# Kernel optimization log

Hardware: AMD Instinct MI355X
Metric: run time of the kernel (lower is better)

The kernel has to match this reference:

```python
import jax, jax.numpy as jnp
import numpy as np

EMB = 1024
NH = 16
T = 2048
B = 2

def setup_inputs() -> dict:
    key = jax.random.key(0)
    k1, k2, k3, k4, k5 = jax.random.split(key, 5)
    s = 0.02
    return {
        "x": jax.random.normal(k1, (B, T, EMB), dtype=jnp.float32),
        "W_attn": jax.random.normal(k2, (EMB, 3 * EMB), dtype=jnp.float32) * s,
        "b_attn": jax.random.normal(k3, (3 * EMB,), dtype=jnp.float32) * s,
        "W_proj": jax.random.normal(k4, (EMB, EMB), dtype=jnp.float32) * s,
        "b_proj": jax.random.normal(k5, (EMB,), dtype=jnp.float32) * s,
    }

def reference(x, W_attn, b_attn, W_proj, b_proj):
    Bz, Tz, C = x.shape
    hd = C // NH
    qkv = x @ W_attn + b_attn                      # [B,T,3C]
    q, k, v = jnp.split(qkv, 3, axis=-1)
    # [B,T,C] -> [B,H,T,hd]
    def heads(t):
        return t.reshape(Bz, Tz, NH, hd).transpose(0, 2, 1, 3)
    q, k, v = heads(q), heads(k), heads(v)
    scale = 1.0 / jnp.sqrt(jnp.float32(hd))
    att = jnp.einsum("bhqd,bhkd->bhqk", q, k) * scale   # [B,H,T,T]
    causal = jnp.tril(jnp.ones((Tz, Tz), dtype=bool))
    att = jnp.where(causal, att, jnp.finfo(att.dtype).min)
    att = jax.nn.softmax(att, axis=-1)
    y = jnp.einsum("bhqk,bhkd->bhqd", att, v)            # [B,H,T,hd]
    y = y.transpose(0, 2, 1, 3).reshape(Bz, Tz, C)
    return y @ W_proj + b_proj
```

## Files before the change

### kernel.cpp

```cpp
#include <hip/hip_runtime.h>
#include <cstdint>
#include <cstddef>

typedef _Float16 half8 __attribute__((ext_vector_type(8)));
typedef _Float16 half4v __attribute__((ext_vector_type(4)));
typedef float f32x4 __attribute__((ext_vector_type(4)));
typedef int int4v __attribute__((ext_vector_type(4)));

#define EMBD 1024
#define NHEAD 16
#define TSEQ 2048
#define NB 2
#define HD 64
#define NBH (NB*NHEAD)
#define SCK 0.18033688f

static __device__ __forceinline__ void gload_lds16(const void* g, void* l) {
    __builtin_amdgcn_global_load_lds((const __attribute__((address_space(1))) void*)g,
                                     (__attribute__((address_space(3))) void*)l,
                                     16, 0, 0);
}

static __device__ __forceinline__ int pk2(float a, float b) {
    return __builtin_bit_cast(int, __builtin_amdgcn_cvt_pkrtz(a, b));
}

__global__ __launch_bounds__(256) void k_prep(
    const float* __restrict__ x,  _Float16* __restrict__ xh,
    const float* __restrict__ Wa, const float* __restrict__ Wp,
    _Float16* __restrict__ WaT,   _Float16* __restrict__ WpT)
{
    const int bx = blockIdx.x;
    if (bx < 4096) {
        int i = bx * 256 + threadIdx.x;
        float4 v = ((const float4*)x)[i];
        half4v h;
        h.x = (_Float16)v.x; h.y = (_Float16)v.y; h.z = (_Float16)v.z; h.w = (_Float16)v.w;
        ((half4v*)xh)[i] = h;
        return;
    }
    __shared__ float tile[32][33];
    const int idx = bx - 4096;
    const int bxx = idx & 127;
    const int byy = idx >> 7;
    const bool isA = bxx < 96;
    const float* in  = isA ? Wa : Wp;
    _Float16* out    = isA ? WaT : WpT;
    const int C      = isA ? 3072 : 1024;
    const int c0 = (isA ? bxx : bxx - 96) * 32, r0 = byy * 32;
    const int tx = threadIdx.x & 31, ty = threadIdx.x >> 5;
    #pragma unroll
    for (int j = 0; j < 4; ++j)
        tile[ty + 8*j][tx] = in[(size_t)(r0 + ty + 8*j) * C + c0 + tx];
    __syncthreads();
    #pragma unroll
    for (int j = 0; j < 4; ++j)
        out[(size_t)(c0 + ty + 8*j) * 1024 + r0 + tx] = (_Float16)tile[tx][ty + 8*j];
}

__global__ __launch_bounds__(256) void k_gemm_qkv(
    const _Float16* __restrict__ A,
    const _Float16* __restrict__ Bt,
    const float* __restrict__ bias,
    _Float16* __restrict__ outq,
    _Float16* __restrict__ VT)
{
    __shared__ _Float16 smem[12288];
    _Float16* As = smem;
    _Float16* Bs = smem + 8192;

    const int d    = blockIdx.x;
    const int xcd  = d & 7;
    const int idx  = d >> 3;
    const int mt   = (xcd >> 1) * 8  + (idx & 7);
    const int ntl  = (xcd &  1) * 24 + (idx >> 3);
    const int m0 = mt * 128, n0 = ntl * 64;

    const int tid  = threadIdx.x;
    const int lane = tid & 63;
    const int w    = tid >> 6;
    const int wm   = w >> 1, wn = w & 1;
    const int l15  = lane & 15;
    const int lg   = lane >> 4;

    f32x4 acc[4][2];
    #pragma unroll
    for (int i = 0; i < 4; ++i) {
        acc[i][0] = (f32x4){0.f, 0.f, 0.f, 0.f};
        acc[i][1] = (f32x4){0.f, 0.f, 0.f, 0.f};
    }

    for (int kt = 0; kt < 16; ++kt) {
        __syncthreads();
        #pragma unroll
        for (int c = 0; c < 4; ++c) {
            int s = c * 256 + tid;
            int r = s >> 3, sl = s & 7;
            const _Float16* ga = A + (size_t)(m0 + r) * 1024 + kt * 64 + ((sl ^ (r & 7)) * 8);
            gload_lds16(ga, (char*)As + s * 16);
        }
        #pragma unroll
        for (int c = 0; c < 2; ++c) {
            int s = c * 256 + tid;
            int r = s >> 3, sl = s & 7;
            const _Float16* gb = Bt + (size_t)(n0 + r) * 1024 + kt * 64 + ((sl ^ (r & 7)) * 8);
            gload_lds16(gb, (char*)Bs + s * 16);
        }
        __syncthreads();

        half8 af[4][2], bf[2][2];
        #pragma unroll
        for (int mf = 0; mf < 4; ++mf) {
            int r = wm * 64 + mf * 16 + l15;
            #pragma unroll
            for (int ks = 0; ks < 2; ++ks)
                af[mf][ks] = *(const half8*)((const char*)As + r * 128 + (((ks * 4 + lg) ^ (r & 7)) * 16));
        }
        #pragma unroll
        for (int nf = 0; nf < 2; ++nf) {
            int r = wn * 32 + nf * 16 + l15;
            #pragma unroll
            for (int ks = 0; ks < 2; ++ks)
                bf[nf][ks] = *(const half8*)((const char*)Bs + r * 128 + (((ks * 4 + lg) ^ (r & 7)) * 16));
        }
        #pragma unroll
        for (int mf = 0; mf < 4; ++mf)
            #pragma unroll
            for (int nf = 0; nf < 2; ++nf) {
                acc[mf][nf] = __builtin_amdgcn_mfma_f32_16x16x32_f16(af[mf][0], bf[nf][0], acc[mf][nf], 0, 0, 0);
                acc[mf][nf] = __builtin_amdgcn_mfma_f32_16x16x32_f16(af[mf][1], bf[nf][1], acc[mf][nf], 0, 0, 0);
            }
    }

    float bv[2];
    bv[0] = bias[n0 + wn * 32 + l15];
    bv[1] = bias[n0 + wn * 32 + 16 + l15];

    const int which = n0 >> 10;
    if (which < 2) {
        const float osc = (which == 1) ? SCK : 1.0f;
        #pragma unroll
        for (int mf = 0; mf < 4; ++mf) {
            #pragma unroll
            for (int j = 0; j < 4; ++j) {
                int m = m0 + wm * 64 + mf * 16 + lg * 4 + j;
                _Float16* po = outq + (size_t)m * 3072 + n0 + wn * 32 + l15;
                po[0]  = (_Float16)((acc[mf][0][j] + bv[0]) * osc);
                po[16] = (_Float16)((acc[mf][1][j] + bv[1]) * osc);
            }
        }
    } else {
        __syncthreads();
        #pragma unroll
        for (int mf = 0; mf < 4; ++mf)
            #pragma unroll
            for (int j = 0; j < 4; ++j) {
                int m = wm * 64 + mf * 16 + lg * 4 + j;
                smem[m * 65 + wn * 32 + l15]      = (_Float16)(acc[mf][0][j] + bv[0]);
                smem[m * 65 + wn * 32 + 16 + l15] = (_Float16)(acc[mf][1][j] + bv[1]);
            }
        __syncthreads();

        const int b     = m0 >> 11;
        const int h     = (n0 - 2048) >> 6;
        const int tloc0 = m0 & 2047;
        _Float16* vbase = VT + ((size_t)(b * 16 + h) * 64) * 2048 + tloc0;
        #pragma unroll
        for (int c = 0; c < 4; ++c) {
            int seg = c * 256 + tid;
            int dd  = seg >> 4;
            int s   = seg & 15;
            half8 hv8;
            #pragma unroll
            for (int e = 0; e < 8; ++e) {
                int p = s * 8 + e;
                int k = 16 * (2 * (p >> 5) + ((p & 7) >> 2)) + 4 * ((p >> 3) & 3) + (p & 3);
                hv8[e] = smem[k * 65 + dd];
            }
            *(half8*)&vbase[(size_t)dd * 2048 + s * 8] = hv8;
        }
    }
}

__global__ __launch_bounds__(256) void k_gemm_proj(
    const _Float16* __restrict__ A,
    const _Float16* __restrict__ Bt,
    const float* __restrict__ bias,
    float* __restrict__ outf)
{
    __shared__ _Float16 As[64 * 64];
    __shared__ _Float16 Bs[128 * 64];

    const int d   = blockIdx.x;
    const int xcd = d & 7;
    const int idx = d >> 3;
    const int mt  = (xcd >> 1) * 16 + (idx & 15);
    const int nt  = (xcd &  1) * 4  + (idx >> 4);
    const int m0 = mt * 64, n0 = nt * 128;

    const int tid  = threadIdx.x;
    const int lane = tid & 63;
    const int wn   = tid >> 6;
    const int l15  = lane & 15;
    const int lg   = lane >> 4;

    f32x4 acc[4][2];
    #pragma unroll
    for (int i = 0; i < 4; ++i) {
        acc[i][0] = (f32x4){0.f, 0.f, 0.f, 0.f};
        acc[i][1] = (f32x4){0.f, 0.f, 0.f, 0.f};
    }

    for (int kt = 0; kt < 16; ++kt) {
        __syncthreads();
        #pragma unroll
        for (int c = 0; c < 2; ++c) {
            int s = c * 256 + tid;
            int r = s >> 3, sl = s & 7;
            const _Float16* ga = A + (size_t)(m0 + r) * 1024 + kt * 64 + ((sl ^ (r & 7)) * 8);
            gload_lds16(ga, (char*)As + s * 16);
        }
        #pragma unroll
        for (int c = 0; c < 4; ++c) {
            int s = c * 256 + tid;
            int r = s >> 3, sl = s & 7;
            const _Float16* gb = Bt + (size_t)(n0 + r) * 1024 + kt * 64 + ((sl ^ (r & 7)) * 8);
            gload_lds16(gb, (char*)Bs + s * 16);
        }
        __syncthreads();

        half8 af[4][2], bf[2][2];
        #pragma unroll
        for (int mf = 0; mf < 4; ++mf) {
            int r = mf * 16 + l15;
            #pragma unroll
            for (int ks = 0; ks < 2; ++ks)
                af[mf][ks] = *(const half8*)((const char*)As + r * 128 + (((ks * 4 + lg) ^ (r & 7)) * 16));
        }
        #pragma unroll
        for (int nf = 0; nf < 2; ++nf) {
            int r = wn * 32 + nf * 16 + l15;
            #pragma unroll
            for (int ks = 0; ks < 2; ++ks)
                bf[nf][ks] = *(const half8*)((const char*)Bs + r * 128 + (((ks * 4 + lg) ^ (r & 7)) * 16));
        }
        #pragma unroll
        for (int mf = 0; mf < 4; ++mf)
            #pragma unroll
            for (int nf = 0; nf < 2; ++nf) {
                acc[mf][nf] = __builtin_amdgcn_mfma_f32_16x16x32_f16(af[mf][0], bf[nf][0], acc[mf][nf], 0, 0, 0);
                acc[mf][nf] = __builtin_amdgcn_mfma_f32_16x16x32_f16(af[mf][1], bf[nf][1], acc[mf][nf], 0, 0, 0);
            }
    }

    float bv[2];
    bv[0] = bias[n0 + wn * 32 + l15];
    bv[1] = bias[n0 + wn * 32 + 16 + l15];

    #pragma unroll
    for (int mf = 0; mf < 4; ++mf) {
        #pragma unroll
        for (int j = 0; j < 4; ++j) {
            int m = m0 + mf * 16 + lg * 4 + j;
            float* po = outf + (size_t)m * 1024 + n0 + wn * 32 + l15;
            po[0]  = acc[mf][0][j] + bv[0];
            po[16] = acc[mf][1][j] + bv[1];
        }
    }
}

__global__ __launch_bounds__(512) void k_attn(
    const _Float16* __restrict__ qkv,
    const _Float16* __restrict__ VTg,
    _Float16* __restrict__ Y)
{
    __shared__ _Float16 Kt[2][8192];
    __shared__ _Float16 Vt[2][8192];

    const int tid  = threadIdx.x;
    const int lane = tid & 63;
    const int w    = tid >> 6;
    const int l15  = lane & 15;
    const int lg   = lane >> 4;
    const int bh   = blockIdx.x;
    const int by   = blockIdx.y;
    const int qt   = (by < 8) ? (15 - by) : (by - 8);
    const int b    = bh >> 4, h = bh & 15;

    const int rA  = tid >> 3;
    const int slA = tid & 7;
    const size_t kOffA = (size_t)rA * 3072 + ((slA ^ (rA & 7)) * 8);
    const _Float16* kBase = qkv + (size_t)(b * 2048) * 3072 + 1024 + h * 64;

    const int dA = tid >> 4;
    const int sA = tid & 15;
    const size_t vOffA = (size_t)dA * 2048 + ((sA ^ (dA & 15)) * 8);
    const _Float16* vBase = VTg + (size_t)bh * TSEQ * HD;

    const int x7   = l15 & 7;
    const int kph0 = (lg ^ x7) * 8;
    const int kph1 = ((4 + lg) ^ x7) * 8;

    const int qrow = qt * 128 + w * 16 + l15;
    const _Float16* qptr = qkv + (size_t)(b * 2048 + qrow) * 3072 + h * 64;
    half8 qa0 = *(const half8*)&qptr[lg * 8];
    half8 qa1 = *(const half8*)&qptr[32 + lg * 8];

    half8 ones;
    #pragma unroll
    for (int i = 0; i < 8; ++i) ones[i] = (_Float16)1.0f;

    f32x4 yac[4];
    #pragma unroll
    for (int nf = 0; nf < 4; ++nf) yac[nf] = (f32x4){0.f, 0.f, 0.f, 0.f};
    f32x4 lsum = (f32x4){0.f, 0.f, 0.f, 0.f};

    const int nkt = qt + 1;

    half8 kra = *(const half8*)(kBase + kOffA);
    half8 krb = *(const half8*)(kBase + kOffA + (size_t)64 * 3072);
    half8 vra = *(const half8*)(vBase + vOffA);
    half8 vrb = *(const half8*)(vBase + vOffA + 32 * 2048);

    for (int kt = 0; kt < nkt; ++kt) {
        const int cur = kt & 1;
        _Float16* KtC = Kt[cur];
        _Float16* VtC = Vt[cur];
        *(half8*)&KtC[tid * 8]        = kra;
        *(half8*)&KtC[4096 + tid * 8] = krb;
        *(half8*)&VtC[tid * 8]        = vra;
        *(half8*)&VtC[4096 + tid * 8] = vrb;
        if (kt + 1 < nkt) {
            const _Float16* kp = kBase + (size_t)(kt + 1) * 128 * 3072;
            kra = *(const half8*)(kp + kOffA);
            krb = *(const half8*)(kp + kOffA + (size_t)64 * 3072);
            const _Float16* vp = vBase + (kt + 1) * 128;
            vra = *(const half8*)(vp + vOffA);
            vrb = *(const half8*)(vp + vOffA + 32 * 2048);
        }
        asm volatile("s_waitcnt lgkmcnt(0)" ::: "memory");
        __builtin_amdgcn_s_barrier();
        __builtin_amdgcn_sched_barrier(0);

        const bool diag = (kt == nkt - 1);

        f32x4 s[8];
        __builtin_amdgcn_s_setprio(1);
        #pragma unroll
        for (int f = 0; f < 8; ++f) {
            if (diag && f > w) { s[f] = (f32x4){0.f, 0.f, 0.f, 0.f}; continue; }
            int rr = f * 16 + l15;
            half8 kb0 = *(const half8*)&KtC[rr * 64 + kph0];
            half8 kb1 = *(const half8*)&KtC[rr * 64 + kph1];
            f32x4 z = (f32x4){0.f, 0.f, 0.f, 0.f};
            z = __builtin_amdgcn_mfma_f32_16x16x32_f16(kb0, qa0, z, 0, 0, 0);
            z = __builtin_amdgcn_mfma_f32_16x16x32_f16(kb1, qa1, z, 0, 0, 0);
            s[f] = z;
        }
        __builtin_amdgcn_s_setprio(0);

        if (diag) {
            const int qg = qt * 128 + w * 16 + l15;
            #pragma unroll
            for (int f = 0; f < 8; ++f) {
                if (f > w) continue;
                #pragma unroll
                for (int j = 0; j < 4; ++j) {
                    int kk = kt * 128 + 16 * f + 4 * lg + j;
                    s[f][j] = (kk > qg) ? 0.f : exp2f(s[f][j]);
                }
            }
        } else {
            #pragma unroll
            for (int f = 0; f < 8; ++f)
                #pragma unroll
                for (int j = 0; j < 4; ++j) s[f][j] = exp2f(s[f][j]);
        }

        __builtin_amdgcn_s_setprio(1);
        #pragma unroll
        for (int t = 0; t < 4; ++t) {
            int4v pi;
            pi[0] = pk2(s[2 * t][0],     s[2 * t][1]);
            pi[1] = pk2(s[2 * t][2],     s[2 * t][3]);
            pi[2] = pk2(s[2 * t + 1][0], s[2 * t + 1][1]);
            pi[3] = pk2(s[2 * t + 1][2], s[2 * t + 1][3]);
            half8 pa = __builtin_bit_cast(half8, pi);
            lsum = __builtin_amdgcn_mfma_f32_16x16x32_f16(pa, ones, lsum, 0, 0, 0);
            #pragma unroll
            for (int nf = 0; nf < 4; ++nf) {
                half8 vb = *(const half8*)&VtC[(nf * 16 + l15) * 128 + (((t * 4 + lg) ^ l15) * 8)];
                yac[nf] = __builtin_amdgcn_mfma_f32_16x16x32_f16(pa, vb, yac[nf], 0, 0, 0);
            }
        }
        __builtin_amdgcn_s_setprio(0);
    }

    const int trow = qt * 128 + w * 16 + lg * 4;
    #pragma unroll
    for (int j = 0; j < 4; ++j) {
        float inv = 1.f / lsum[j];
        #pragma unroll
        for (int nf = 0; nf < 4; ++nf) {
            float yv = yac[nf][j] * inv;
            Y[((size_t)b * TSEQ + trow + j) * EMBD + h * 64 + nf * 16 + l15] = (_Float16)yv;
        }
    }
}

extern "C" void kernel_launch(void* const* d_in, const int* in_sizes, int n_in,
                              void* d_out, int out_size, void* d_ws, size_t ws_size,
                              hipStream_t stream) {
    const float* x  = (const float*)d_in[0];
    const float* Wa = (const float*)d_in[1];
    const float* ba = (const float*)d_in[2];
    const float* Wp = (const float*)d_in[3];
    const float* bp = (const float*)d_in[4];
    float* out = (float*)d_out;

    _Float16* Xh   = (_Float16*)d_ws;
    _Float16* WaT  = Xh   + (size_t)4096 * 1024;
    _Float16* WpT  = WaT  + (size_t)3072 * 1024;
    _Float16* QKVn = WpT  + (size_t)1024 * 1024;
    _Float16* VTb  = QKVn + (size_t)4096 * 3072;
    _Float16* Yh   = Xh;

    k_prep<<<8192, 256, 0, stream>>>(x, Xh, Wa, Wp, WaT, WpT);

    k_gemm_qkv<<<1536, 256, 0, stream>>>(Xh, WaT, ba, QKVn, VTb);

    k_attn<<<dim3(NBH, 16), 512, 0, stream>>>(QKVn, VTb, Yh);

    k_gemm_proj<<<512, 256, 0, stream>>>(Yh, WpT, bp, out);
}
```

Baseline: 95.94 us.

## Compute Q, K and V tiles for one head per block in QKV GEMM

Each QKV GEMM block now loads its A tile once and multiplies it against three B tiles (Q, K and V columns for the same head slice), keeping three accumulator sets. The grid shrinks from 1536 to 512 blocks. This cuts redundant A-tile global loads by a factor of three. In exchange it raises register pressure (96 accumulator floats per thread) and LDS use, and leaves fewer blocks to fill the GPU, which may lower occupancy.

```diff
diff --git a/kernel.cpp b/kernel.cpp
--- a/kernel.cpp
+++ b/kernel.cpp
@@ -65,16 +65,16 @@
     _Float16* __restrict__ outq,
     _Float16* __restrict__ VT)
 {
-    __shared__ _Float16 smem[12288];
+    __shared__ _Float16 smem[20480];
     _Float16* As = smem;
-    _Float16* Bs = smem + 8192;
-
-    const int d    = blockIdx.x;
-    const int xcd  = d & 7;
-    const int idx  = d >> 3;
-    const int mt   = (xcd >> 1) * 8  + (idx & 7);
-    const int ntl  = (xcd &  1) * 24 + (idx >> 3);
-    const int m0 = mt * 128, n0 = ntl * 64;
+
+    const int d   = blockIdx.x;
+    const int xcd = d & 7;
+    const int idx = d >> 3;
+    const int mt  = (xcd >> 1) * 8 + (idx & 7);
+    const int ntl = (xcd &  1) * 8 + (idx >> 3);
+    const int m0 = mt * 128;
+    const int hc = ntl * 64;
 
     const int tid  = threadIdx.x;
     const int lane = tid & 63;
@@ -83,12 +83,14 @@
     const int l15  = lane & 15;
     const int lg   = lane >> 4;
 
-    f32x4 acc[4][2];
-    #pragma unroll
-    for (int i = 0; i < 4; ++i) {
-        acc[i][0] = (f32x4){0.f, 0.f, 0.f, 0.f};
-        acc[i][1] = (f32x4){0.f, 0.f, 0.f, 0.f};
-    }
+    f32x4 acc[3][4][2];
+    #pragma unroll
+    for (int q = 0; q < 3; ++q)
+        #pragma unroll
+        for (int i = 0; i < 4; ++i) {
+            acc[q][i][0] = (f32x4){0.f, 0.f, 0.f, 0.f};
+            acc[q][i][1] = (f32x4){0.f, 0.f, 0.f, 0.f};
+        }
 
     for (int kt = 0; kt < 16; ++kt) {
         __syncthreads();
@@ -100,15 +102,18 @@
             gload_lds16(ga, (char*)As + s * 16);
         }
         #pragma unroll
-        for (int c = 0; c < 2; ++c) {
-            int s = c * 256 + tid;
-            int r = s >> 3, sl = s & 7;
-            const _Float16* gb = Bt + (size_t)(n0 + r) * 1024 + kt * 64 + ((sl ^ (r & 7)) * 8);
-            gload_lds16(gb, (char*)Bs + s * 16);
-        }
-        __syncthreads();
-
-        half8 af[4][2], bf[2][2];
+        for (int q = 0; q < 3; ++q) {
+            #pragma unroll
+            for (int c = 0; c < 2; ++c) {
+                int s = c * 256 + tid;
+                int r = s >> 3, sl = s & 7;
+                const _Float16* gb = Bt + (size_t)(q * 1024 + hc + r) * 1024 + kt * 64 + ((sl ^ (r & 7)) * 8);
+                gload_lds16(gb, (char*)(smem + 8192 + q * 4096) + s * 16);
+            }
+        }
+        __syncthreads();
+
+        half8 af[4][2];
         #pragma unroll
         for (int mf = 0; mf < 4; ++mf) {
             int r = wm * 64 + mf * 16 + l15;
@@ -117,54 +122,59 @@
                 af[mf][ks] = *(const half8*)((const char*)As + r * 128 + (((ks * 4 + lg) ^ (r & 7)) * 16));
         }
         #pragma unroll
-        for (int nf = 0; nf < 2; ++nf) {
-            int r = wn * 32 + nf * 16 + l15;
-            #pragma unroll
-            for (int ks = 0; ks < 2; ++ks)
-                bf[nf][ks] = *(const half8*)((const char*)Bs + r * 128 + (((ks * 4 + lg) ^ (r & 7)) * 16));
-        }
-        #pragma unroll
-        for (int mf = 0; mf < 4; ++mf)
+        for (int q = 0; q < 3; ++q) {
+            const char* BsQ = (const char*)(smem + 8192 + q * 4096);
+            half8 bf[2][2];
             #pragma unroll
             for (int nf = 0; nf < 2; ++nf) {
-                acc[mf][nf] = __builtin_amdgcn_mfma_f32_16x16x32_f16(af[mf][0], bf[nf][0], acc[mf][nf], 0, 0, 0);
-                acc[mf][nf] = __builtin_amdgcn_mfma_f32_16x16x32_f16(af[mf][1], bf[nf][1], acc[mf][nf], 0, 0, 0);
-            }
-    }
-
-    float bv[2];
-    bv[0] = bias[n0 + wn * 32 + l15];
-    bv[1] = bias[n0 + wn * 32 + 16 + l15];
-
-    const int which = n0 >> 10;
-    if (which < 2) {
-        const float osc = (which == 1) ? SCK : 1.0f;
+                int r = wn * 32 + nf * 16 + l15;
+                #pragma unroll
+                for (int ks = 0; ks < 2; ++ks)
+                    bf[nf][ks] = *(const half8*)(BsQ + r * 128 + (((ks * 4 + lg) ^ (r & 7)) * 16));
+            }
+            #pragma unroll
+            for (int mf = 0; mf < 4; ++mf)
+                #pragma unroll
+                for (int nf = 0; nf < 2; ++nf) {
+                    acc[q][mf][nf] = __builtin_amdgcn_mfma_f32_16x16x32_f16(af[mf][0], bf[nf][0], acc[q][mf][nf], 0, 0, 0);
+                    acc[q][mf][nf] = __builtin_amdgcn_mfma_f32_16x16x32_f16(af[mf][1], bf[nf][1], acc[q][mf][nf], 0, 0, 0);
+                }
+        }
+    }
+
+    #pragma unroll
+    for (int q = 0; q < 2; ++q) {
+        float bv0 = bias[q * 1024 + hc + wn * 32 + l15];
+        float bv1 = bias[q * 1024 + hc + wn * 32 + 16 + l15];
+        const float osc = (q == 1) ? SCK : 1.0f;
         #pragma unroll
         for (int mf = 0; mf < 4; ++mf) {
             #pragma unroll
             for (int j = 0; j < 4; ++j) {
                 int m = m0 + wm * 64 + mf * 16 + lg * 4 + j;
-                _Float16* po = outq + (size_t)m * 3072 + n0 + wn * 32 + l15;
-                po[0]  = (_Float16)((acc[mf][0][j] + bv[0]) * osc);
-                po[16] = (_Float16)((acc[mf][1][j] + bv[1]) * osc);
-            }
-        }
-    } else {
+                _Float16* po = outq + (size_t)m * 3072 + q * 1024 + hc + wn * 32 + l15;
+                po[0]  = (_Float16)((acc[q][mf][0][j] + bv0) * osc);
+                po[16] = (_Float16)((acc[q][mf][1][j] + bv1) * osc);
+            }
+        }
+    }
+    {
+        float bv0 = bias[2048 + hc + wn * 32 + l15];
+        float bv1 = bias[2048 + hc + wn * 32 + 16 + l15];
         __syncthreads();
         #pragma unroll
         for (int mf = 0; mf < 4; ++mf)
             #pragma unroll
             for (int j = 0; j < 4; ++j) {
                 int m = wm * 64 + mf * 16 + lg * 4 + j;
-                smem[m * 65 + wn * 32 + l15]      = (_Float16)(acc[mf][0][j] + bv[0]);
-                smem[m * 65 + wn * 32 + 16 + l15] = (_Float16)(acc[mf][1][j] + bv[1]);
+                smem[m * 65 + wn * 32 + l15]      = (_Float16)(acc[2][mf][0][j] + bv0);
+                smem[m * 65 + wn * 32 + 16 + l15] = (_Float16)(acc[2][mf][1][j] + bv1);
             }
         __syncthreads();
 
         const int b     = m0 >> 11;
-        const int h     = (n0 - 2048) >> 6;
         const int tloc0 = m0 & 2047;
-        _Float16* vbase = VT + ((size_t)(b * 16 + h) * 64) * 2048 + tloc0;
+        _Float16* vbase = VT + ((size_t)(b * 16 + ntl) * 64) * 2048 + tloc0;
         #pragma unroll
         for (int c = 0; c < 4; ++c) {
             int seg = c * 256 + tid;
@@ -427,7 +437,7 @@
 
     k_prep<<<8192, 256, 0, stream>>>(x, Xh, Wa, Wp, WaT, WpT);
 
-    k_gemm_qkv<<<1536, 256, 0, stream>>>(Xh, WaT, ba, QKVn, VTb);
+    k_gemm_qkv<<<512, 256, 0, stream>>>(Xh, WaT, ba, QKVn, VTb);
 
     k_attn<<<dim3(NBH, 16), 512, 0, stream>>>(QKVn, VTb, Yh);
 
```

After: 94.87 us. No clear change (-1.1%).
